# Performance work log

Hardware: AMD Instinct MI355X
Metric: run time of the kernel (lower is better)

The kernel has to match this reference:

```python
import jax, jax.numpy as jnp
import numpy as np
import math

B, S, D, H = 2, 2048, 1024, 16


def setup_inputs() -> dict:
    key = jax.random.key(0)
    ks = jax.random.split(key, 5)
    sc = 0.02  # small init scale for weights
    return {
        "x": jax.random.normal(ks[0], (B, S, D), dtype=jnp.float32),
        "Wqkv_w": jax.random.normal(ks[1], (3 * D, D), dtype=jnp.float32) * sc,
        "Wqkv_b": jnp.zeros((3 * D,), jnp.float32),
        "sel_w": jax.random.normal(ks[2], (1, D), dtype=jnp.float32) * sc,
        "sel_b": jnp.zeros((1,), jnp.float32),
        "out_w": jax.random.normal(ks[3], (D, D), dtype=jnp.float32) * sc,
        "out_b": jnp.zeros((D,), jnp.float32),
    }


def reference(x, Wqkv_w, Wqkv_b, sel_w, sel_b, out_w, out_b):
    b, s, d = x.shape
    h = H
    hd = d // h
    # Wqkv projection -> (b, s, 3, h, hd)
    qkv = (x @ Wqkv_w.T + Wqkv_b).reshape(b, s, 3, h, hd)
    q, k, v = qkv[:, :, 0], qkv[:, :, 1], qkv[:, :, 2]
    scale = 1.0 / math.sqrt(hd)
    scores = jnp.einsum('bthd,bshd->bhts', q, k * scale)  # (b,h,s,s)
    causal_mask = jnp.triu(jnp.full((s, s), -10000.0, dtype=scores.dtype), 1)
    attn = jax.nn.softmax(scores + causal_mask, axis=-1)
    ctx = jnp.einsum('bhts,bshd->bthd', attn, v).reshape(b, s, d)
    attn_out = ctx @ out_w.T + out_b  # (b,s,d)
    # selection: softmax over sequence dim, scaled by sqrt(d)/8
    sel = jax.nn.softmax(x @ sel_w.T + sel_b, axis=1) * (math.sqrt(d) / 8.0)  # (b,s,1)
    # eval path: topk over sequence, gather, scatter_add into x
    kk = math.ceil(math.sqrt(s))  # 46 for s=2048
    _, idx = jax.lax.top_k(sel[..., 0], kk)  # (b,kk) indices into seq dim
    val = attn_out * sel  # (b,s,d)
    bidx = jnp.arange(b)[:, None]
    src = val[bidx, idx]  # gather -> (b,kk,d)
    y = x.at[bidx, idx].add(src)  # scatter_add
    return y
```

## Files before the change

### kernel.cpp

```cpp
#include <hip/hip_runtime.h>
#include <stdint.h>

#define BATCH 2
#define SEQ   2048
#define DIM   1024
#define NH    16
#define HD    64
#define KK    46
#define NSEL  (BATCH*KK)
#define MPAD  128
#define CHUNK 128
#define NCH   (SEQ/CHUNK)
#define QP    48
#define SPLITK 8

typedef __attribute__((ext_vector_type(8))) short short8;
typedef __attribute__((ext_vector_type(4))) float f32x4;

__device__ inline unsigned short f2bf(float f) {
  union { float f; uint32_t u; } v; v.f = f;
  uint32_t u = v.u;
  uint32_t r = u + 0x7fff + ((u >> 16) & 1);
  return (unsigned short)(r >> 16);
}
__device__ inline float bf2f(unsigned short h) {
  union { uint32_t u; float f; } v; v.u = ((uint32_t)h) << 16;
  return v.f;
}
__device__ inline uint32_t f2ord(float f) {
  union { float f; uint32_t u; } v; v.f = f;
  return (v.u & 0x80000000u) ? ~v.u : (v.u | 0x80000000u);
}

__device__ inline void gload16(const void* g, void* l) {
  __builtin_amdgcn_global_load_lds(
      (const __attribute__((address_space(1))) void*)g,
      (__attribute__((address_space(3))) void*)l, 16, 0, 0);
}

__global__ __launch_bounds__(256) void prep_kernel(
    const float* __restrict__ wqkv, const float* __restrict__ outw,
    unsigned short* __restrict__ wqkvb, unsigned short* __restrict__ outwb,
    const float* __restrict__ x, unsigned short* __restrict__ xb,
    const float* __restrict__ sel_w, const float* __restrict__ sel_b,
    float* __restrict__ z, float* __restrict__ out)
{
  if (blockIdx.x < 2048) {
    int i = (blockIdx.x * 256 + threadIdx.x) * 8;
    const int NW = 3 * DIM * DIM;
    const float* src; unsigned short* dst; int j;
    if (i < NW) { src = wqkv; dst = wqkvb; j = i; }
    else        { src = outw; dst = outwb; j = i - NW; }
    float4 a = *(const float4*)(src + j);
    float4 b = *(const float4*)(src + j + 4);
    ushort4 o0, o1;
    o0.x = f2bf(a.x); o0.y = f2bf(a.y); o0.z = f2bf(a.z); o0.w = f2bf(a.w);
    o1.x = f2bf(b.x); o1.y = f2bf(b.y); o1.z = f2bf(b.z); o1.w = f2bf(b.w);
    *(ushort4*)(dst + j)     = o0;
    *(ushort4*)(dst + j + 4) = o1;
  } else {
    int wave = threadIdx.x >> 6, lane = threadIdx.x & 63;
    int row = (blockIdx.x - 2048) * 4 + wave;
    const float* xr = x + (size_t)row * DIM;
    unsigned short* xo = xb + (size_t)row * DIM;
    float* oo = out + (size_t)row * DIM;
    float s = 0.f;
#pragma unroll
    for (int it = 0; it < 4; ++it) {
      int c = it * 256 + lane * 4;
      float4 xv = *(const float4*)(xr + c);
      float4 wv = *(const float4*)(sel_w + c);
      s += xv.x*wv.x + xv.y*wv.y + xv.z*wv.z + xv.w*wv.w;
      ushort4 o;
      o.x = f2bf(xv.x); o.y = f2bf(xv.y); o.z = f2bf(xv.z); o.w = f2bf(xv.w);
      *(ushort4*)(xo + c) = o;
      *(float4*)(oo + c) = xv;
    }
#pragma unroll
    for (int o = 32; o > 0; o >>= 1) s += __shfl_xor(s, o);
    if (lane == 0) z[row] = s + sel_b[0];
  }
}

__global__ __launch_bounds__(256) void topk_kernel(const float* __restrict__ z,
                                                   float* __restrict__ sel,
                                                   int* __restrict__ idxout)
{
  int b = blockIdx.x, t = threadIdx.x;
  int lane = t & 63, wid = t >> 6;
  __shared__ int   hist[256];
  __shared__ float fred[4];
  __shared__ int   ired[4];
  __shared__ int   s_B, s_need;
  __shared__ float s_mx, s_sum;

  int s0 = t * 8;
  float zz[8];
  uint32_t uu[8];
  {
    float4 a = *(const float4*)(z + b*SEQ + s0);
    float4 c = *(const float4*)(z + b*SEQ + s0 + 4);
    zz[0]=a.x; zz[1]=a.y; zz[2]=a.z; zz[3]=a.w;
    zz[4]=c.x; zz[5]=c.y; zz[6]=c.z; zz[7]=c.w;
  }
#pragma unroll
  for (int i = 0; i < 8; ++i) uu[i] = f2ord(zz[i]);

  float lm = zz[0];
#pragma unroll
  for (int i = 1; i < 8; ++i) lm = fmaxf(lm, zz[i]);
#pragma unroll
  for (int o = 32; o > 0; o >>= 1) lm = fmaxf(lm, __shfl_xor(lm, o));
  if (lane == 0) fred[wid] = lm;
  __syncthreads();
  if (t == 0) s_mx = fmaxf(fmaxf(fred[0], fred[1]), fmaxf(fred[2], fred[3]));
  __syncthreads();
  float mx = s_mx;

  float pp[8];
  float ls = 0.f;
#pragma unroll
  for (int i = 0; i < 8; ++i) { pp[i] = __expf(zz[i] - mx); ls += pp[i]; }
#pragma unroll
  for (int o = 32; o > 0; o >>= 1) ls += __shfl_xor(ls, o);
  if (lane == 0) fred[wid] = ls;
  __syncthreads();
  if (t == 0) s_sum = fred[0] + fred[1] + fred[2] + fred[3];
  __syncthreads();
  float sscale = 4.0f / s_sum;
#pragma unroll
  for (int i = 0; i < 8; ++i) sel[b*SEQ + s0 + i] = pp[i] * sscale;

  uint32_t pref = 0;
  int need = KK;
#pragma unroll
  for (int pass = 0; pass < 4; ++pass) {
    int shift = 24 - pass * 8;
    uint32_t maskhi = pass ? (0xFFFFFFFFu << (shift + 8)) : 0u;
    hist[t] = 0;
    __syncthreads();
#pragma unroll
    for (int i = 0; i < 8; ++i) {
      if ((uu[i] & maskhi) == pref)
        atomicAdd(&hist[(uu[i] >> shift) & 255], 1);
    }
    __syncthreads();
    if (t < 64) {
      int c0 = hist[t*4], c1 = hist[t*4+1], c2 = hist[t*4+2], c3 = hist[t*4+3];
      int sl = c0 + c1 + c2 + c3;
      int suf = sl;
#pragma unroll
      for (int off = 1; off < 64; off <<= 1) {
        int o = __shfl_down(suf, off);
        if (lane + off < 64) suf += o;
      }
      int above = suf - sl;
      if (above < need && above + sl >= need) {
        int cum = above;
        int cs[4] = {c0, c1, c2, c3};
#pragma unroll
        for (int k = 3; k >= 0; --k) {
          if (cum < need && cum + cs[k] >= need) {
            s_B = t*4 + k;
            s_need = need - cum;
            break;
          }
          cum += cs[k];
        }
      }
    }
    __syncthreads();
    pref |= ((uint32_t)s_B) << shift;
    need = s_need;
    __syncthreads();
  }
  uint32_t T = pref;

  int cgt = 0, ceq = 0;
#pragma unroll
  for (int i = 0; i < 8; ++i) { cgt += (uu[i] > T); ceq += (uu[i] == T); }
  int pack = (cgt << 12) | ceq;
  int inc = pack;
#pragma unroll
  for (int off = 1; off < 64; off <<= 1) {
    int o = __shfl_up(inc, off);
    if (lane >= off) inc += o;
  }
  if (lane == 63) ired[wid] = inc;
  __syncthreads();
  int wbase = 0;
  if (wid == 1) wbase = ired[0];
  else if (wid == 2) wbase = ired[0] + ired[1];
  else if (wid == 3) wbase = ired[0] + ired[1] + ired[2];
  int ex = wbase + inc - pack;
  int g = ex >> 12, e = ex & 0xFFF;
#pragma unroll
  for (int i = 0; i < 8; ++i) {
    int s = s0 + i;
    bool isgt = uu[i] > T;
    bool iseq = uu[i] == T;
    int rank = -1;
    if (isgt) rank = g + (e < need ? e : need);
    else if (iseq && e < need) rank = g + e;
    if (rank >= 0) idxout[b*KK + rank] = s;
    g += isgt; e += iseq;
  }
}

__global__ __launch_bounds__(256) void gemms_kernel(
    const unsigned short* __restrict__ xb,
    const unsigned short* __restrict__ wqkvb,
    const float* __restrict__ Wqkv_b,
    unsigned short* __restrict__ kvb,
    float* __restrict__ qpart,
    const int* __restrict__ idxp)
{
  __shared__ unsigned short As[3][128*32];
  __shared__ unsigned short Bs[3][128*32];
  int tid  = threadIdx.x;
  int lane = tid & 63, wave = tid >> 6;
  int wr = (wave >> 1) * 64, wc = (wave & 1) * 64;
  int lr = lane & 15;
  int sx = (((lane >> 4) ^ ((lane >> 1) & 3)) << 3);
  int srow = lane >> 2;
  int scol = (((lane & 3) ^ ((lane >> 3) & 3)) << 3);
  int rb = 4 * (lane >> 4);

  if (blockIdx.x < 512) {
    const unsigned short* Bw = wqkvb + (size_t)DIM * DIM;
    int flat = blockIdx.x;
    int xcd = flat & 7, i8 = flat >> 3;
    int tile = xcd * 64 + i8;
    int bx = tile & 15, by = tile >> 4;
    int bm = by * 128, bn = bx * 128;
    const int K = DIM, N = 2 * DIM, nt = 32;

    const unsigned short* ap[2];
    const unsigned short* bp[2];
#pragma unroll
    for (int c = 0; c < 2; ++c) {
      int row = (wave * 2 + c) * 16 + srow;
      ap[c] = xb + (size_t)(bm + row) * K + scol;
      bp[c] = Bw + (size_t)(bn + row) * K + scol;
    }
    f32x4 acc[4][4] = {};
#pragma unroll
    for (int pb = 0; pb < 2; ++pb) {
#pragma unroll
      for (int c = 0; c < 2; ++c) {
        int ch = wave * 2 + c;
        gload16(ap[c], (char*)As[pb] + ch * 1024 + lane * 16);
        gload16(bp[c], (char*)Bs[pb] + ch * 1024 + lane * 16);
        ap[c] += 32; bp[c] += 32;
      }
    }
    int cur = 0;
    for (int t = 0; t < nt; ++t) {
      if (t + 1 < nt) asm volatile("s_waitcnt vmcnt(4)" ::: "memory");
      else            asm volatile("s_waitcnt vmcnt(0)" ::: "memory");
      __builtin_amdgcn_s_barrier();
      asm volatile("" ::: "memory");
      __builtin_amdgcn_sched_barrier(0);
      short8 af[4], bf[4];
#pragma unroll
      for (int m = 0; m < 4; ++m) af[m] = *(const short8*)&As[cur][(wr + m*16 + lr)*32 + sx];
#pragma unroll
      for (int n = 0; n < 4; ++n) bf[n] = *(const short8*)&Bs[cur][(wc + n*16 + lr)*32 + sx];
      if (t + 2 < nt) {
        int nb = cur + 2; if (nb >= 3) nb -= 3;
#pragma unroll
        for (int c = 0; c < 2; ++c) {
          int ch = wave * 2 + c;
          gload16(ap[c], (char*)As[nb] + ch * 1024 + lane * 16);
          gload16(bp[c], (char*)Bs[nb] + ch * 1024 + lane * 16);
          ap[c] += 32; bp[c] += 32;
        }
      }
#pragma unroll
      for (int m = 0; m < 4; ++m)
#pragma unroll
        for (int n = 0; n < 4; ++n)
          acc[m][n] = __builtin_amdgcn_mfma_f32_16x16x32_bf16(af[m], bf[n], acc[m][n], 0, 0, 0);
      cur = (cur + 1 == 3) ? 0 : cur + 1;
    }
#pragma unroll
    for (int m = 0; m < 4; ++m) {
#pragma unroll
      for (int n = 0; n < 4; ++n) {
        int col = bn + wc + n*16 + lr;
        float bv = Wqkv_b[DIM + col];
#pragma unroll
        for (int i = 0; i < 4; ++i) {
          int row = bm + wr + m*16 + rb + i;
          kvb[(size_t)row * N + col] = f2bf(acc[m][n][i] + bv);
        }
      }
    }
  } else {
    int bi = blockIdx.x - 512;
    int sk = bi >> 3;
    int bn = (bi & 7) * 128;
    int kb = sk * 128;
    const int K = DIM, N = DIM, nt = 4;

    const unsigned short* ap[2];
    const unsigned short* bp[2];
#pragma unroll
    for (int c = 0; c < 2; ++c) {
      int row = (wave * 2 + c) * 16 + srow;
      int bb = 0, rr = 0;
      if (row < NSEL) { bb = row / KK; rr = idxp[row]; }
      ap[c] = xb + ((size_t)(bb * SEQ + rr)) * K + kb + scol;
      bp[c] = wqkvb + (size_t)(bn + row) * K + kb + scol;
    }
    f32x4 acc[4][4] = {};
#pragma unroll
    for (int pb = 0; pb < 2; ++pb) {
#pragma unroll
      for (int c = 0; c < 2; ++c) {
        int ch = wave * 2 + c;
        gload16(ap[c], (char*)As[pb] + ch * 1024 + lane * 16);
        gload16(bp[c], (char*)Bs[pb] + ch * 1024 + lane * 16);
        ap[c] += 32; bp[c] += 32;
      }
    }
    int cur = 0;
    for (int t = 0; t < nt; ++t) {
      if (t + 1 < nt) asm volatile("s_waitcnt vmcnt(4)" ::: "memory");
      else            asm volatile("s_waitcnt vmcnt(0)" ::: "memory");
      __builtin_amdgcn_s_barrier();
      asm volatile("" ::: "memory");
      __builtin_amdgcn_sched_barrier(0);
      short8 af[4], bf[4];
#pragma unroll
      for (int m = 0; m < 4; ++m) af[m] = *(const short8*)&As[cur][(wr + m*16 + lr)*32 + sx];
#pragma unroll
      for (int n = 0; n < 4; ++n) bf[n] = *(const short8*)&Bs[cur][(wc + n*16 + lr)*32 + sx];
      if (t + 2 < nt) {
        int nb = cur + 2; if (nb >= 3) nb -= 3;
#pragma unroll
        for (int c = 0; c < 2; ++c) {
          int ch = wave * 2 + c;
          gload16(ap[c], (char*)As[nb] + ch * 1024 + lane * 16);
          gload16(bp[c], (char*)Bs[nb] + ch * 1024 + lane * 16);
          ap[c] += 32; bp[c] += 32;
        }
      }
#pragma unroll
      for (int m = 0; m < 4; ++m)
#pragma unroll
        for (int n = 0; n < 4; ++n)
          acc[m][n] = __builtin_amdgcn_mfma_f32_16x16x32_bf16(af[m], bf[n], acc[m][n], 0, 0, 0);
      cur = (cur + 1 == 3) ? 0 : cur + 1;
    }
    float* po = qpart + (size_t)sk * MPAD * N;
#pragma unroll
    for (int m = 0; m < 4; ++m) {
#pragma unroll
      for (int n = 0; n < 4; ++n) {
        int col = bn + wc + n*16 + lr;
#pragma unroll
        for (int i = 0; i < 4; ++i) {
          int row = wr + m*16 + rb + i;
          po[(size_t)row * N + col] = acc[m][n][i];
        }
      }
    }
  }
}

__global__ __launch_bounds__(256) void gemm_splitk_kernel(
    const unsigned short* __restrict__ A,
    const unsigned short* __restrict__ Bw,
    float* __restrict__ part, int N, int K)
{
  __shared__ unsigned short As[3][128*32];
  __shared__ unsigned short Bs[3][128*32];
  int tid  = threadIdx.x;
  int lane = tid & 63, wave = tid >> 6;
  int wr = (wave >> 1) * 64, wc = (wave & 1) * 64;
  int bn = blockIdx.x * 128;
  int sk = blockIdx.z;
  int ksl = K / SPLITK;
  int kb  = sk * ksl;

  int lr = lane & 15;
  int sx = (((lane >> 4) ^ ((lane >> 1) & 3)) << 3);
  int srow = lane >> 2;
  int scol = (((lane & 3) ^ ((lane >> 3) & 3)) << 3);

  const unsigned short* ap[2];
  const unsigned short* bp[2];
#pragma unroll
  for (int c = 0; c < 2; ++c) {
    int row = (wave * 2 + c) * 16 + srow;
    ap[c] = A  + (size_t)row * K + kb + scol;
    bp[c] = Bw + (size_t)(bn + row) * K + kb + scol;
  }

  f32x4 acc[4][4] = {};
  const int nt = 4;
#pragma unroll
  for (int pb = 0; pb < 2; ++pb) {
#pragma unroll
    for (int c = 0; c < 2; ++c) {
      int ch = wave * 2 + c;
      gload16(ap[c], (char*)As[pb] + ch * 1024 + lane * 16);
      gload16(bp[c], (char*)Bs[pb] + ch * 1024 + lane * 16);
      ap[c] += 32; bp[c] += 32;
    }
  }
  int cur = 0;
  for (int t = 0; t < nt; ++t) {
    if (t + 1 < nt) asm volatile("s_waitcnt vmcnt(4)" ::: "memory");
    else            asm volatile("s_waitcnt vmcnt(0)" ::: "memory");
    __builtin_amdgcn_s_barrier();
    asm volatile("" ::: "memory");
    __builtin_amdgcn_sched_barrier(0);
    short8 af[4], bf[4];
#pragma unroll
    for (int m = 0; m < 4; ++m) af[m] = *(const short8*)&As[cur][(wr + m*16 + lr)*32 + sx];
#pragma unroll
    for (int n = 0; n < 4; ++n) bf[n] = *(const short8*)&Bs[cur][(wc + n*16 + lr)*32 + sx];
    if (t + 2 < nt) {
      int nb = cur + 2; if (nb >= 3) nb -= 3;
#pragma unroll
      for (int c = 0; c < 2; ++c) {
        int ch = wave * 2 + c;
        gload16(ap[c], (char*)As[nb] + ch * 1024 + lane * 16);
        gload16(bp[c], (char*)Bs[nb] + ch * 1024 + lane * 16);
        ap[c] += 32; bp[c] += 32;
      }
    }
#pragma unroll
    for (int m = 0; m < 4; ++m)
#pragma unroll
      for (int n = 0; n < 4; ++n)
        acc[m][n] = __builtin_amdgcn_mfma_f32_16x16x32_bf16(af[m], bf[n], acc[m][n], 0, 0, 0);
    cur = (cur + 1 == 3) ? 0 : cur + 1;
  }

  int rb = 4 * (lane >> 4);
  float* po = part + (size_t)sk * MPAD * N;
#pragma unroll
  for (int m = 0; m < 4; ++m) {
#pragma unroll
    for (int n = 0; n < 4; ++n) {
      int col = bn + wc + n*16 + lr;
#pragma unroll
      for (int i = 0; i < 4; ++i) {
        int row = wr + m*16 + rb + i;
        po[(size_t)row * N + col] = acc[m][n][i];
      }
    }
  }
}

__global__ __launch_bounds__(256) void attn_chunk_kernel(
    const float* __restrict__ qpart,
    const float* __restrict__ Wqkv_b,
    const unsigned short* __restrict__ kvb,
    const int* __restrict__ idx,
    float* __restrict__ Opart,
    float* __restrict__ mpart,
    float* __restrict__ lpart)
{
  int h = blockIdx.x, b = blockIdx.y, kc = blockIdx.z;
  int t = threadIdx.x, lane = t & 63, w = t >> 6;
  int lr = lane & 15, hk = lane >> 4;

  __shared__ unsigned short Qs[QP][72];
  __shared__ union { unsigned short Ks[CHUNK][72]; unsigned short ps[QP][136]; } U;
  __shared__ unsigned short Vt[HD][134];
  __shared__ int   rsi[QP];
  __shared__ float wred[4][QP];
  __shared__ float wsum[4][QP];

  if (t < QP) rsi[t] = (t < KK) ? idx[b*KK + t] : -1;
  for (int i = t; i < QP*8; i += 256) {
    int q = i >> 3, c8 = (i & 7) * 8;
    if (q < KK) {
      int j = b*KK + q;
      float4 b0 = *(const float4*)(Wqkv_b + h*HD + c8);
      float4 b1 = *(const float4*)(Wqkv_b + h*HD + c8 + 4);
      float v0 = b0.x, v1 = b0.y, v2 = b0.z, v3 = b0.w;
      float v4 = b1.x, v5 = b1.y, v6 = b1.z, v7 = b1.w;
#pragma unroll
      for (int sk = 0; sk < SPLITK; ++sk) {
        const float* p = qpart + ((size_t)sk * MPAD + j) * DIM + h*HD + c8;
        float4 a0 = *(const float4*)p;
        float4 a1 = *(const float4*)(p + 4);
        v0 += a0.x; v1 += a0.y; v2 += a0.z; v3 += a0.w;
        v4 += a1.x; v5 += a1.y; v6 += a1.z; v7 += a1.w;
      }
      Qs[q][c8+0] = f2bf(v0); Qs[q][c8+1] = f2bf(v1);
      Qs[q][c8+2] = f2bf(v2); Qs[q][c8+3] = f2bf(v3);
      Qs[q][c8+4] = f2bf(v4); Qs[q][c8+5] = f2bf(v5);
      Qs[q][c8+6] = f2bf(v6); Qs[q][c8+7] = f2bf(v7);
    } else {
      uint4 zz; zz.x = 0; zz.y = 0; zz.z = 0; zz.w = 0;
      *(uint4*)&Qs[q][c8] = zz;
    }
  }
  for (int i = t; i < CHUNK*8; i += 256) {
    int r = i >> 3, c8 = (i & 7) * 8;
    *(uint4*)&U.Ks[r][c8] =
      *(const uint4*)(kvb + ((size_t)(b*SEQ + kc*CHUNK + r))*2048 + h*HD + c8);
  }
  for (int i = t; i < CHUNK*8; i += 256) {
    int r = i >> 3, d8 = (i & 7) * 8;
    uint4 v = *(const uint4*)(kvb + ((size_t)(b*SEQ + kc*CHUNK + r))*2048 + DIM + h*HD + d8);
    const unsigned short* pv = (const unsigned short*)&v;
#pragma unroll
    for (int j = 0; j < 8; ++j) Vt[d8 + j][r] = pv[j];
  }
  __syncthreads();

  short8 af[3][2], bfr[2][2];
#pragma unroll
  for (int m = 0; m < 3; ++m)
#pragma unroll
    for (int kk = 0; kk < 2; ++kk)
      af[m][kk] = *(const short8*)&Qs[m*16 + lr][kk*32 + hk*8];
#pragma unroll
  for (int j = 0; j < 2; ++j)
#pragma unroll
    for (int kk = 0; kk < 2; ++kk)
      bfr[j][kk] = *(const short8*)&U.Ks[(2*w + j)*16 + lr][kk*32 + hk*8];
  f32x4 acc[3][2] = {};
#pragma unroll
  for (int kk = 0; kk < 2; ++kk)
#pragma unroll
    for (int m = 0; m < 3; ++m)
#pragma unroll
      for (int j = 0; j < 2; ++j)
        acc[m][j] = __builtin_amdgcn_mfma_f32_16x16x32_bf16(af[m][kk], bfr[j][kk], acc[m][j], 0, 0, 0);

  float s[3][2][4];
  float rmax[3][4];
#pragma unroll
  for (int m = 0; m < 3; ++m)
#pragma unroll
    for (int reg = 0; reg < 4; ++reg) {
      int row = m*16 + hk*4 + reg;
      int rq = rsi[row];
      float mx = -3e38f;
#pragma unroll
      for (int j = 0; j < 2; ++j) {
        int gkey = kc*CHUNK + (2*w + j)*16 + lr;
        float v = acc[m][j][reg] * 0.125f;
        if (gkey > rq) v = -3e38f;
        s[m][j][reg] = v;
        mx = fmaxf(mx, v);
      }
#pragma unroll
      for (int o = 1; o < 16; o <<= 1) mx = fmaxf(mx, __shfl_xor(mx, o));
      rmax[m][reg] = mx;
    }
  if (lr == 0) {
#pragma unroll
    for (int m = 0; m < 3; ++m)
#pragma unroll
      for (int reg = 0; reg < 4; ++reg)
        wred[w][m*16 + hk*4 + reg] = rmax[m][reg];
  }
  __syncthreads();

  float rsum[3][4];
#pragma unroll
  for (int m = 0; m < 3; ++m)
#pragma unroll
    for (int reg = 0; reg < 4; ++reg) {
      int row = m*16 + hk*4 + reg;
      float gm = fmaxf(fmaxf(wred[0][row], wred[1][row]), fmaxf(wred[2][row], wred[3][row]));
      gm = fmaxf(gm, -1e37f);
      float sum = 0.f;
#pragma unroll
      for (int j = 0; j < 2; ++j) {
        float p = __expf(s[m][j][reg] - gm);
        sum += p;
        U.ps[row][(2*w + j)*16 + lr] = f2bf(p);
      }
#pragma unroll
      for (int o = 1; o < 16; o <<= 1) sum += __shfl_xor(sum, o);
      rsum[m][reg] = sum;
      rmax[m][reg] = gm;
    }
  if (lr == 0) {
#pragma unroll
    for (int m = 0; m < 3; ++m)
#pragma unroll
      for (int reg = 0; reg < 4; ++reg)
        wsum[w][m*16 + hk*4 + reg] = rsum[m][reg];
  }
  __syncthreads();

  if (w == 0 && lr == 0) {
    size_t base = ((size_t)(b*NH + h)*NCH + kc)*KK;
#pragma unroll
    for (int m = 0; m < 3; ++m)
#pragma unroll
      for (int reg = 0; reg < 4; ++reg) {
        int row = m*16 + hk*4 + reg;
        if (row < KK) {
          float L = wsum[0][row] + wsum[1][row] + wsum[2][row] + wsum[3][row];
          mpart[base + row] = rmax[m][reg];
          lpart[base + row] = L;
        }
      }
  }

  f32x4 acc2[3] = {};
#pragma unroll
  for (int kt = 0; kt < 4; ++kt) {
    short8 bv = *(const short8*)&Vt[w*16 + lr][kt*32 + hk*8];
#pragma unroll
    for (int m = 0; m < 3; ++m) {
      short8 av = *(const short8*)&U.ps[m*16 + lr][kt*32 + hk*8];
      acc2[m] = __builtin_amdgcn_mfma_f32_16x16x32_bf16(av, bv, acc2[m], 0, 0, 0);
    }
  }
  size_t obase = (((size_t)(b*NH + h)*NCH + kc)*KK)*HD;
#pragma unroll
  for (int m = 0; m < 3; ++m)
#pragma unroll
    for (int reg = 0; reg < 4; ++reg) {
      int q = m*16 + hk*4 + reg;
      if (q < KK) Opart[obase + (size_t)q*HD + w*16 + lr] = acc2[m][reg];
    }
}

__global__ __launch_bounds__(64) void attn_combine_kernel(
    const float* __restrict__ Opart,
    const float* __restrict__ mpart,
    const float* __restrict__ lpart,
    unsigned short* __restrict__ ctxg)
{
  int h = blockIdx.x, j = blockIdx.y;
  int b = j / KK, q = j % KK;
  int d = threadIdx.x;
  size_t mb = (size_t)(b*NH + h)*NCH;
  float M = -3e38f;
#pragma unroll
  for (int c = 0; c < NCH; ++c) M = fmaxf(M, mpart[(mb + c)*KK + q]);
  float L = 0.f, o = 0.f;
#pragma unroll
  for (int c = 0; c < NCH; ++c) {
    float f = __expf(mpart[(mb + c)*KK + q] - M);
    L += lpart[(mb + c)*KK + q] * f;
    o = fmaf(Opart[((mb + c)*KK + q)*HD + d], f, o);
  }
  ctxg[(size_t)j*DIM + h*HD + d] = f2bf(o / L);
}

__global__ void rowfix_kernel(const float* __restrict__ x,
                              const float* __restrict__ apart,
                              const float* __restrict__ out_b,
                              const float* __restrict__ sel,
                              const int* __restrict__ idx,
                              float* __restrict__ out)
{
  int j = blockIdx.x;
  int b = j / KK;
  int r = idx[j];
  int col = threadIdx.x * 4;
  size_t off = ((size_t)(b * SEQ + r)) * DIM + col;
  float s = sel[b * SEQ + r];
  float4 a = *(const float4*)(out_b + col);
#pragma unroll
  for (int sk = 0; sk < SPLITK; ++sk) {
    float4 p = *(const float4*)(apart + ((size_t)sk * MPAD + j) * DIM + col);
    a.x += p.x; a.y += p.y; a.z += p.z; a.w += p.w;
  }
  float4 v = *(const float4*)(x + off);
  v.x += a.x * s; v.y += a.y * s; v.z += a.z * s; v.w += a.w * s;
  *(float4*)(out + off) = v;
}

extern "C" void kernel_launch(void* const* d_in, const int* in_sizes, int n_in,
                              void* d_out, int out_size, void* d_ws, size_t ws_size,
                              hipStream_t stream)
{
  (void)in_sizes; (void)n_in; (void)out_size; (void)ws_size;
  const float* x      = (const float*)d_in[0];
  const float* Wqkv_w = (const float*)d_in[1];
  const float* Wqkv_b = (const float*)d_in[2];
  const float* sel_w  = (const float*)d_in[3];
  const float* sel_b  = (const float*)d_in[4];
  const float* out_w  = (const float*)d_in[5];
  const float* out_b  = (const float*)d_in[6];
  float* out = (float*)d_out;
  char* ws = (char*)d_ws;

  unsigned short* xb    = (unsigned short*)(ws);
  unsigned short* wqkvb = (unsigned short*)(ws + (8u  << 20));
  unsigned short* outwb = (unsigned short*)(ws + (14u << 20));
  unsigned short* kvb   = (unsigned short*)(ws + (16u << 20));
  float* z      = (float*)(ws + (32u << 20));
  float* sel    = (float*)(ws + (32u << 20) + (16u << 10));
  int*   idx    = (int*)  (ws + (32u << 20) + (32u << 10));
  unsigned short* ctxg = (unsigned short*)(ws + (33u << 20) + (256u << 10));
  float* Opart = (float*)(ws + (35u << 20));
  float* mpart = (float*)(ws + (42u << 20));
  float* lpart = (float*)(ws + (42u << 20) + (256u << 10));
  float* qpart = (float*)(ws + (44u << 20));
  float* apart = (float*)(ws + (48u << 20));

  prep_kernel<<<3072, 256, 0, stream>>>(Wqkv_w, out_w, wqkvb, outwb,
                                        x, xb, sel_w, sel_b, z, out);
  topk_kernel<<<BATCH, 256, 0, stream>>>(z, sel, idx);

  gemms_kernel<<<576, 256, 0, stream>>>(xb, wqkvb, Wqkv_b, kvb, qpart, idx);

  dim3 gac(NH, BATCH, NCH);
  attn_chunk_kernel<<<gac, 256, 0, stream>>>(qpart, Wqkv_b, kvb, idx, Opart, mpart, lpart);
  dim3 gcb(NH, NSEL);
  attn_combine_kernel<<<gcb, 64, 0, stream>>>(Opart, mpart, lpart, ctxg);

  dim3 gsk(DIM/128, 1, SPLITK);
  gemm_splitk_kernel<<<gsk, 256, 0, stream>>>(ctxg, outwb, apart, DIM, DIM);

  rowfix_kernel<<<NSEL, 256, 0, stream>>>(x, apart, out_b, sel, idx, out);
}
```

Before: 69.90 us.

## Fuse attention split-combine into the out-projection split-K GEMM prologue

Removes the separate attn_combine kernel and the bf16 ctx buffer. Each split-K GEMM block now merges the per-chunk partial outputs, maxima and sums for its two heads directly into a padded LDS A tile, then runs the MFMA loop with only the weight tiles streamed from memory. This saves one kernel launch and a global round trip. In exchange, every one of the 8 column blocks redundantly recomputes the same combine, and each thread holds 64 float accumulators, which raises register pressure and adds prologue latency to the GEMM.

Measured after the change: 99.95 us. +43.0%, slower.

```diff
diff --git a/kernel.cpp b/kernel.cpp
--- a/kernel.cpp
+++ b/kernel.cpp
@@ -370,56 +370,92 @@
 }
 
 __global__ __launch_bounds__(256) void gemm_splitk_kernel(
-    const unsigned short* __restrict__ A,
+    const float* __restrict__ Opart,
+    const float* __restrict__ mpart,
+    const float* __restrict__ lpart,
     const unsigned short* __restrict__ Bw,
-    float* __restrict__ part, int N, int K)
+    float* __restrict__ part)
 {
-  __shared__ unsigned short As[3][128*32];
+  __shared__ unsigned short ASf[128][136];
   __shared__ unsigned short Bs[3][128*32];
   int tid  = threadIdx.x;
   int lane = tid & 63, wave = tid >> 6;
   int wr = (wave >> 1) * 64, wc = (wave & 1) * 64;
   int bn = blockIdx.x * 128;
   int sk = blockIdx.z;
-  int ksl = K / SPLITK;
-  int kb  = sk * ksl;
-
-  int lr = lane & 15;
-  int sx = (((lane >> 4) ^ ((lane >> 1) & 3)) << 3);
+  int kb  = sk * 128;
+  const int K = DIM, N = DIM, nt = 4;
+
+  int lr = lane & 15, hk8 = (lane >> 4) * 8;
   int srow = lane >> 2;
   int scol = (((lane & 3) ^ ((lane >> 3) & 3)) << 3);
-
-  const unsigned short* ap[2];
+  int sx = (((lane >> 4) ^ ((lane >> 1) & 3)) << 3);
+
   const unsigned short* bp[2];
 #pragma unroll
   for (int c = 0; c < 2; ++c) {
     int row = (wave * 2 + c) * 16 + srow;
-    ap[c] = A  + (size_t)row * K + kb + scol;
     bp[c] = Bw + (size_t)(bn + row) * K + kb + scol;
   }
-
-  f32x4 acc[4][4] = {};
-  const int nt = 4;
 #pragma unroll
   for (int pb = 0; pb < 2; ++pb) {
 #pragma unroll
     for (int c = 0; c < 2; ++c) {
       int ch = wave * 2 + c;
-      gload16(ap[c], (char*)As[pb] + ch * 1024 + lane * 16);
       gload16(bp[c], (char*)Bs[pb] + ch * 1024 + lane * 16);
-      ap[c] += 32; bp[c] += 32;
-    }
-  }
+      bp[c] += 32;
+    }
+  }
+
+  {
+    int j = tid & 127, half = tid >> 7;
+    int h = (kb >> 6) + half;
+    if (j < NSEL) {
+      int b = j / KK, q = j - b * KK;
+      size_t mb = (size_t)(b * NH + h) * NCH;
+      float M = -3e38f;
+#pragma unroll
+      for (int c = 0; c < NCH; ++c) M = fmaxf(M, mpart[(mb + c) * KK + q]);
+      float o[64];
+#pragma unroll
+      for (int d = 0; d < 64; ++d) o[d] = 0.f;
+      float L = 0.f;
+#pragma unroll
+      for (int c = 0; c < NCH; ++c) {
+        float f = __expf(mpart[(mb + c) * KK + q] - M);
+        L += lpart[(mb + c) * KK + q] * f;
+        const float* op = Opart + ((mb + c) * KK + q) * HD;
+#pragma unroll
+        for (int d4 = 0; d4 < 16; ++d4) {
+          float4 v = *(const float4*)(op + d4 * 4);
+          o[d4*4+0] = fmaf(v.x, f, o[d4*4+0]);
+          o[d4*4+1] = fmaf(v.y, f, o[d4*4+1]);
+          o[d4*4+2] = fmaf(v.z, f, o[d4*4+2]);
+          o[d4*4+3] = fmaf(v.w, f, o[d4*4+3]);
+        }
+      }
+      float inv = 1.f / L;
+#pragma unroll
+      for (int d = 0; d < 64; ++d)
+        ASf[j][half * 64 + d] = f2bf(o[d] * inv);
+    } else {
+#pragma unroll
+      for (int d = 0; d < 64; ++d) ASf[j][half * 64 + d] = 0;
+    }
+  }
+  asm volatile("s_waitcnt lgkmcnt(0)" ::: "memory");
+
+  f32x4 acc[4][4] = {};
   int cur = 0;
   for (int t = 0; t < nt; ++t) {
-    if (t + 1 < nt) asm volatile("s_waitcnt vmcnt(4)" ::: "memory");
+    if (t + 1 < nt) asm volatile("s_waitcnt vmcnt(2)" ::: "memory");
     else            asm volatile("s_waitcnt vmcnt(0)" ::: "memory");
     __builtin_amdgcn_s_barrier();
     asm volatile("" ::: "memory");
     __builtin_amdgcn_sched_barrier(0);
     short8 af[4], bf[4];
 #pragma unroll
-    for (int m = 0; m < 4; ++m) af[m] = *(const short8*)&As[cur][(wr + m*16 + lr)*32 + sx];
+    for (int m = 0; m < 4; ++m) af[m] = *(const short8*)&ASf[wr + m*16 + lr][t*32 + hk8];
 #pragma unroll
     for (int n = 0; n < 4; ++n) bf[n] = *(const short8*)&Bs[cur][(wc + n*16 + lr)*32 + sx];
     if (t + 2 < nt) {
@@ -427,9 +463,8 @@
 #pragma unroll
       for (int c = 0; c < 2; ++c) {
         int ch = wave * 2 + c;
-        gload16(ap[c], (char*)As[nb] + ch * 1024 + lane * 16);
         gload16(bp[c], (char*)Bs[nb] + ch * 1024 + lane * 16);
-        ap[c] += 32; bp[c] += 32;
+        bp[c] += 32;
       }
     }
 #pragma unroll
@@ -628,29 +663,6 @@
       int q = m*16 + hk*4 + reg;
       if (q < KK) Opart[obase + (size_t)q*HD + w*16 + lr] = acc2[m][reg];
     }
-}
-
-__global__ __launch_bounds__(64) void attn_combine_kernel(
-    const float* __restrict__ Opart,
-    const float* __restrict__ mpart,
-    const float* __restrict__ lpart,
-    unsigned short* __restrict__ ctxg)
-{
-  int h = blockIdx.x, j = blockIdx.y;
-  int b = j / KK, q = j % KK;
-  int d = threadIdx.x;
-  size_t mb = (size_t)(b*NH + h)*NCH;
-  float M = -3e38f;
-#pragma unroll
-  for (int c = 0; c < NCH; ++c) M = fmaxf(M, mpart[(mb + c)*KK + q]);
-  float L = 0.f, o = 0.f;
-#pragma unroll
-  for (int c = 0; c < NCH; ++c) {
-    float f = __expf(mpart[(mb + c)*KK + q] - M);
-    L += lpart[(mb + c)*KK + q] * f;
-    o = fmaf(Opart[((mb + c)*KK + q)*HD + d], f, o);
-  }
-  ctxg[(size_t)j*DIM + h*HD + d] = f2bf(o / L);
 }
 
 __global__ void rowfix_kernel(const float* __restrict__ x,
@@ -699,7 +711,6 @@
   float* z      = (float*)(ws + (32u << 20));
   float* sel    = (float*)(ws + (32u << 20) + (16u << 10));
   int*   idx    = (int*)  (ws + (32u << 20) + (32u << 10));
-  unsigned short* ctxg = (unsigned short*)(ws + (33u << 20) + (256u << 10));
   float* Opart = (float*)(ws + (35u << 20));
   float* mpart = (float*)(ws + (42u << 20));
   float* lpart = (float*)(ws + (42u << 20) + (256u << 10));
@@ -714,11 +725,9 @@
 
   dim3 gac(NH, BATCH, NCH);
   attn_chunk_kernel<<<gac, 256, 0, stream>>>(qpart, Wqkv_b, kvb, idx, Opart, mpart, lpart);
-  dim3 gcb(NH, NSEL);
-  attn_combine_kernel<<<gcb, 64, 0, stream>>>(Opart, mpart, lpart, ctxg);
 
   dim3 gsk(DIM/128, 1, SPLITK);
-  gemm_splitk_kernel<<<gsk, 256, 0, stream>>>(ctxg, outwb, apart, DIM, DIM);
+  gemm_splitk_kernel<<<gsk, 256, 0, stream>>>(Opart, mpart, lpart, outwb, apart);
 
   rowfix_kernel<<<NSEL, 256, 0, stream>>>(x, apart, out_b, sel, idx, out);
 }
```
